# Kernel tuning notes

Measured on AMD Instinct MI355X. Metric: run time of the kernel, lower is better.

The kernel has to match this reference:

```python
import jax, jax.numpy as jnp
import numpy as np

EPS = 1e-5  # torch BatchNorm default eps


def _bn_relu(x, g, b, relu):
    # Training-mode BatchNorm1d over (N, C, L): stats over axes (0, 2).
    m = jnp.mean(x, axis=(0, 2), keepdims=True)
    v = jnp.var(x, axis=(0, 2), keepdims=True)
    y = (x - m) * jax.lax.rsqrt(v + EPS) * g[None, :, None] + b[None, :, None]
    return jax.nn.relu(y) if relu else y


def setup_inputs() -> dict:
    key = jax.random.key(0)
    k0, k1, k2 = jax.random.split(key, 3)
    N, C, H = 256, 512, 64  # batch, channels (inplanes==planes), spatial positions (mask_channel)
    x = jax.random.normal(k0, (N, C, H), dtype=jnp.float32)
    # LocallyConnected2d weights: torch shape (1, out, in, H, 1, k^2=1) -> (out, in, H)
    w1 = jax.random.normal(k1, (C, C, H), dtype=jnp.float32) * 0.02
    w2 = jax.random.normal(k2, (C, C, H), dtype=jnp.float32) * 0.02
    g1 = jnp.ones((C,), jnp.float32)
    b1 = jnp.zeros((C,), jnp.float32)
    g2 = jnp.ones((C,), jnp.float32)
    b2 = jnp.zeros((C,), jnp.float32)
    return {"x": x, "w1": w1, "g1": g1, "b1": b1, "w2": w2, "g2": g2, "b2": b2}


def reference(x, w1, g1, b1, w2, g2, b2):
    # conv1: locally-connected 1x1 -> per-position matmul over channels
    out = jnp.einsum('nch,och->noh', x, w1)          # (N, C, H)
    out = _bn_relu(out, g1, b1, relu=True)
    # conv2
    out = jnp.einsum('nch,och->noh', out, w2)
    out = _bn_relu(out, g2, b2, relu=False)
    # residual add (downsample is None) + final relu
    return jax.nn.relu(out + x)
```

## Files before the change

### kernel.cpp

```cpp
#include <hip/hip_runtime.h>
#include <stdint.h>

typedef float  f32x4  __attribute__((ext_vector_type(4)));
typedef __bf16 bf16x8 __attribute__((ext_vector_type(8)));
typedef __bf16 bf16x4 __attribute__((ext_vector_type(4)));

#define N_ 256
#define C_ 512
#define H_ 64
#define RS_ 32768

__device__ __forceinline__ uint32_t pack_bf16x2(float a, float b) {
  const uint16_t ua = __builtin_bit_cast(uint16_t, (__bf16)a);
  const uint16_t ub = __builtin_bit_cast(uint16_t, (__bf16)b);
  return (uint32_t)ua | ((uint32_t)ub << 16);
}

__global__ __launch_bounds__(256) void k_prep(const float* __restrict__ x,
                                              const float* __restrict__ w1,
                                              const float* __restrict__ w2,
                                              __bf16* __restrict__ xT,
                                              __bf16* __restrict__ w1T,
                                              __bf16* __restrict__ w2T,
                                              float* __restrict__ stats) {
  __shared__ uint32_t tile[256][33];
  const int t  = threadIdx.x;
  const int by = blockIdx.y;
  if (by == 0 && blockIdx.x == 0) {
#pragma unroll
    for (int i = 0; i < 8; ++i) stats[i * 256 + t] = 0.f;
  }
  const float* src;
  __bf16* dst;
  int p;
  if (by < 256)      { src = x;  dst = xT;  p = by; }
  else if (by < 768) { src = w1; dst = w1T; p = by - 256; }
  else               { src = w2; dst = w2T; p = by - 768; }
  const int ch0 = blockIdx.x * 256;
  const float* sbase = src + ((size_t)p * 512 + ch0) * 64;

#pragma unroll
  for (int j = 0; j < 16; ++j) {
    const int fidx = j * 256 + t;
    const int c = fidx >> 4, hq = fidx & 15;
    const float4 v = *reinterpret_cast<const float4*>(sbase + c * 64 + hq * 4);
    tile[c][hq * 2]     = pack_bf16x2(v.x, v.y);
    tile[c][hq * 2 + 1] = pack_bf16x2(v.z, v.w);
  }
  __syncthreads();

  __bf16* dbase = dst + (size_t)p * RS_ + ch0;
#pragma unroll
  for (int j = 0; j < 8; ++j) {
    const int ci = j * 256 + t;
    const int cb = ci & 31, h = ci >> 5;
    const int hm = h >> 1;
    const bool odd = (h & 1) != 0;
    uint32_t W[8];
#pragma unroll
    for (int i = 0; i < 8; ++i) W[i] = tile[cb * 8 + i][hm];
    uint4 o;
    uint32_t* op = reinterpret_cast<uint32_t*>(&o);
#pragma unroll
    for (int k = 0; k < 4; ++k) {
      const uint32_t wa = W[2 * k], wb = W[2 * k + 1];
      op[k] = odd ? ((wa >> 16) | (wb & 0xFFFF0000u))
                  : ((wa & 0xFFFFu) | (wb << 16));
    }
    *reinterpret_cast<uint4*>(dbase + (size_t)h * 512 + cb * 8) = o;
  }
}

template <bool BN_A>
__global__ __launch_bounds__(256, 2) void k_gemm(
    const __bf16* __restrict__ A,
    const __bf16* __restrict__ B,
    __bf16* __restrict__ Co,
    const float* __restrict__ sum_in, const float* __restrict__ sq_in,
    const float* __restrict__ g, const float* __restrict__ bb,
    float* __restrict__ sum_out, float* __restrict__ sq_out) {
  const int wkid = (blockIdx.x & 7) * 64 + (blockIdx.x >> 3);
  const int h  = wkid >> 3;
  const int tm = (wkid >> 2) & 1, tn = wkid & 3;
  const int m0 = tm * 128, n0 = tn * 128;
  const __bf16* Ah = A + (size_t)m0 * RS_ + (size_t)h * C_;
  const __bf16* Bh = B + (size_t)n0 * RS_ + (size_t)h * C_;
  __shared__ __bf16 As[2][128 * 64];
  __shared__ __bf16 Bs[2][128 * 64];
  __shared__ float a_lds[512], c_lds[512];
  const int tid  = threadIdx.x;
  const int lane = tid & 63, wid = tid >> 6;
  const int wr = wid >> 1, wc = wid & 1;
  const int lrow8 = lane >> 3;
  const int swz   = (lane & 7) ^ lrow8;

  if (BN_A) {
#pragma unroll
    for (int ch = tid; ch < 512; ch += 256) {
      const float m    = sum_in[ch] * (1.f / 16384.f);
      const float var  = fmaxf(0.f, sq_in[ch] * (1.f / 16384.f) - m * m);
      const float aa   = g[ch] * rsqrtf(var + 1e-5f);
      a_lds[ch] = aa;
      c_lds[ch] = bb[ch] - m * aa;
    }
    __syncthreads();
  }

  auto stage_b = [&](int buf, int kt) {
#pragma unroll
    for (int i = 0; i < 4; ++i) {
      const int rbase = wid * 32 + i * 8;
      const __bf16* gb = Bh + (size_t)(rbase + lrow8) * RS_ + kt * 64 + swz * 8;
      __builtin_amdgcn_global_load_lds(
          (const __attribute__((address_space(1))) void*)gb,
          (__attribute__((address_space(3))) void*)(&Bs[buf][rbase * 64]), 16, 0, 0);
    }
  };
  auto stage_a = [&](int buf, int kt) {
#pragma unroll
    for (int i = 0; i < 4; ++i) {
      const int rbase = wid * 32 + i * 8;
      const __bf16* ga = Ah + (size_t)(rbase + lrow8) * RS_ + kt * 64 + swz * 8;
      __builtin_amdgcn_global_load_lds(
          (const __attribute__((address_space(1))) void*)ga,
          (__attribute__((address_space(3))) void*)(&As[buf][rbase * 64]), 16, 0, 0);
    }
  };
  const int lr32 = tid >> 3, cch = tid & 7;
  auto load_a = [&](bf16x8* v, int kt) {
#pragma unroll
    for (int i = 0; i < 4; ++i)
      v[i] = *reinterpret_cast<const bf16x8*>(
          Ah + (size_t)(i * 32 + lr32) * RS_ + kt * 64 + cch * 8);
  };
  auto bn_write = [&](const bf16x8* v, int buf, int kt) {
    const int cg = kt * 64 + cch * 8;
    const f32x4 s0 = *reinterpret_cast<const f32x4*>(&a_lds[cg]);
    const f32x4 s1 = *reinterpret_cast<const f32x4*>(&a_lds[cg + 4]);
    const f32x4 h0 = *reinterpret_cast<const f32x4*>(&c_lds[cg]);
    const f32x4 h1 = *reinterpret_cast<const f32x4*>(&c_lds[cg + 4]);
#pragma unroll
    for (int i = 0; i < 4; ++i) {
      const int row = i * 32 + lr32;
      bf16x8 y;
#pragma unroll
      for (int e = 0; e < 4; ++e) {
        y[e]     = (__bf16)fmaxf(0.f, fmaf((float)v[i][e],     s0[e], h0[e]));
        y[e + 4] = (__bf16)fmaxf(0.f, fmaf((float)v[i][e + 4], s1[e], h1[e]));
      }
      const int boff = row * 128 + ((cch * 16) ^ ((row & 7) << 4));
      *reinterpret_cast<bf16x8*>(reinterpret_cast<char*>(&As[buf][0]) + boff) = y;
    }
  };

  f32x4 acc[4][4] = {};
  const int fr = lane & 15, kc = lane >> 4;
  auto compute = [&](int buf) {
#pragma unroll
    for (int kk = 0; kk < 2; ++kk) {
      bf16x8 af[4], bfq[4];
#pragma unroll
      for (int mf = 0; mf < 4; ++mf) {
        const int row  = wr * 64 + mf * 16 + fr;
        const int boff = row * 128 + ((kk * 64 + kc * 16) ^ ((row & 7) << 4));
        af[mf] = *reinterpret_cast<const bf16x8*>(
            reinterpret_cast<const char*>(&As[buf][0]) + boff);
      }
#pragma unroll
      for (int nf = 0; nf < 4; ++nf) {
        const int row  = wc * 64 + nf * 16 + fr;
        const int boff = row * 128 + ((kk * 64 + kc * 16) ^ ((row & 7) << 4));
        bfq[nf] = *reinterpret_cast<const bf16x8*>(
            reinterpret_cast<const char*>(&Bs[buf][0]) + boff);
      }
#pragma unroll
      for (int mf = 0; mf < 4; ++mf)
#pragma unroll
        for (int nf = 0; nf < 4; ++nf)
          acc[mf][nf] = __builtin_amdgcn_mfma_f32_16x16x32_bf16(af[mf], bfq[nf], acc[mf][nf], 0, 0, 0);
    }
  };

  if (BN_A) {
    bf16x8 v0[4];
    load_a(v0, 0);
    bn_write(v0, 0, 0);
  } else {
    stage_a(0, 0);
  }
  stage_b(0, 0);
  __syncthreads();

  int buf = 0;
  for (int kt = 0; kt < 8; ++kt) {
    bf16x8 vn[4];
    if (kt < 7) {
      stage_b(buf ^ 1, kt + 1);
      if (!BN_A) stage_a(buf ^ 1, kt + 1);
      else       load_a(vn, kt + 1);
    }
    compute(buf);
    if (BN_A && kt < 7) bn_write(vn, buf ^ 1, kt + 1);
    __syncthreads();
    buf ^= 1;
  }

  const int rq = (lane >> 4) * 4;
#pragma unroll
  for (int nf = 0; nf < 4; ++nf) {
    const int oc = n0 + wc * 64 + nf * 16 + fr;
    float s = 0.f, s2 = 0.f;
#pragma unroll
    for (int mf = 0; mf < 4; ++mf) {
      const int rb = m0 + wr * 64 + mf * 16 + rq;
      f32x4 v = acc[mf][nf];
#pragma unroll
      for (int j = 0; j < 4; ++j) {
        const float f = v[j];
        Co[(size_t)(rb + j) * RS_ + (size_t)h * C_ + oc] = (__bf16)f;
        s += f;
        s2 += f * f;
      }
    }
    s  += __shfl_xor(s, 16);  s  += __shfl_xor(s, 32);
    s2 += __shfl_xor(s2, 16); s2 += __shfl_xor(s2, 32);
    if (lane < 16) {
      atomicAdd(&sum_out[oc], s);
      atomicAdd(&sq_out[oc], s2);
    }
  }
}

__global__ __launch_bounds__(256) void k_finalize(const __bf16* __restrict__ t2,
                                                  const float* __restrict__ x,
                                                  const float* __restrict__ sum2,
                                                  const float* __restrict__ sq2,
                                                  const float* __restrict__ g2,
                                                  const float* __restrict__ b2,
                                                  float* __restrict__ out) {
  __shared__ float tile[64][65];
  __shared__ float a2s[64], c2s[64];
  const int n  = blockIdx.y;
  const int o0 = blockIdx.x * 64;
  const int t  = threadIdx.x;
  if (t < 64) {
    const int o = o0 + t;
    const float m    = sum2[o] * (1.f / 16384.f);
    const float var  = fmaxf(0.f, sq2[o] * (1.f / 16384.f) - m * m);
    const float a    = g2[o] * rsqrtf(var + 1e-5f);
    a2s[t] = a;
    c2s[t] = b2[o] - m * a;
  }
  const __bf16* tb = t2 + (size_t)n * RS_ + o0;
#pragma unroll
  for (int j = 0; j < 4; ++j) {
    const int hh = j * 16 + (t >> 4);
    const int ol = (t & 15) * 4;
    const bf16x4 v = *reinterpret_cast<const bf16x4*>(tb + (size_t)hh * 512 + ol);
#pragma unroll
    for (int e = 0; e < 4; ++e) tile[hh][ol + e] = (float)v[e];
  }
  __syncthreads();
  const int ol = t >> 2;
  const int hb = (t & 3) * 16;
  const int o  = o0 + ol;
  const float a = a2s[ol], c = c2s[ol];
  const float4* xp = reinterpret_cast<const float4*>(x + ((size_t)n * C_ + o) * H_ + hb);
  float4* op = reinterpret_cast<float4*>(out + ((size_t)n * C_ + o) * H_ + hb);
#pragma unroll
  for (int i4 = 0; i4 < 4; ++i4) {
    const float4 xv = xp[i4];
    float4 r;
    r.x = fmaxf(0.f, fmaf(a, tile[hb + i4 * 4 + 0][ol], c) + xv.x);
    r.y = fmaxf(0.f, fmaf(a, tile[hb + i4 * 4 + 1][ol], c) + xv.y);
    r.z = fmaxf(0.f, fmaf(a, tile[hb + i4 * 4 + 2][ol], c) + xv.z);
    r.w = fmaxf(0.f, fmaf(a, tile[hb + i4 * 4 + 3][ol], c) + xv.w);
    op[i4] = r;
  }
}

extern "C" void kernel_launch(void* const* d_in, const int* in_sizes, int n_in,
                              void* d_out, int out_size, void* d_ws, size_t ws_size,
                              hipStream_t stream) {
  const float* x  = (const float*)d_in[0];
  const float* w1 = (const float*)d_in[1];
  const float* g1 = (const float*)d_in[2];
  const float* b1 = (const float*)d_in[3];
  const float* w2 = (const float*)d_in[4];
  const float* g2 = (const float*)d_in[5];
  const float* b2 = (const float*)d_in[6];
  float* out = (float*)d_out;

  char* ws = (char*)d_ws;
  float* stats = (float*)ws;
  float* sum1 = stats,        *sq1 = stats + 512;
  float* sum2 = stats + 1024, *sq2 = stats + 1536;
  const size_t MB = (size_t)1 << 20;
  __bf16* xT  = (__bf16*)(ws + 64 * 1024);
  __bf16* w1T = (__bf16*)(ws + 64 * 1024 + 16 * MB);
  __bf16* w2T = (__bf16*)(ws + 64 * 1024 + 48 * MB);
  __bf16* t1T = (__bf16*)(ws + 64 * 1024 + 80 * MB);
  __bf16* t2T = (__bf16*)(ws + 64 * 1024 + 96 * MB);

  k_prep<<<dim3(2, 1280), 256, 0, stream>>>(x, w1, w2, xT, w1T, w2T, stats);

  k_gemm<false><<<512, 256, 0, stream>>>(xT, w1T, t1T, nullptr, nullptr,
                                         nullptr, nullptr, sum1, sq1);
  k_gemm<true><<<512, 256, 0, stream>>>(t1T, w2T, t2T, sum1, sq1, g1, b1,
                                        sum2, sq2);

  k_finalize<<<dim3(8, 256), 256, 0, stream>>>(t2T, x, sum2, sq2, g2, b2, out);
}
```

Measured before the change: 107.7 us.

## Restructure prep transpose as persistent per-wave tasks and split GEMM kernels

The prep kernel becomes a grid of 640 blocks whose waves each loop over small 64-channel tasks, staging into a private LDS slice with no block-level barriers. The old version used 2560 blocks with 256-channel tiles and a __syncthreads. The GEMM is moved into a device-function body with two separate wrapper kernels, so the kernel without BN no longer allocates the BN scale LDS arrays. The aim is to cut launch and barrier overhead in the transpose and reduce LDS footprint. The risk is less memory-level parallelism per wave in the prep stage.

```diff
diff --git a/kernel.cpp b/kernel.cpp
--- a/kernel.cpp
+++ b/kernel.cpp
@@ -16,79 +16,79 @@
   return (uint32_t)ua | ((uint32_t)ub << 16);
 }
 
-__global__ __launch_bounds__(256) void k_prep(const float* __restrict__ x,
-                                              const float* __restrict__ w1,
-                                              const float* __restrict__ w2,
-                                              __bf16* __restrict__ xT,
-                                              __bf16* __restrict__ w1T,
-                                              __bf16* __restrict__ w2T,
-                                              float* __restrict__ stats) {
-  __shared__ uint32_t tile[256][33];
-  const int t  = threadIdx.x;
-  const int by = blockIdx.y;
-  if (by == 0 && blockIdx.x == 0) {
+__global__ __launch_bounds__(256) void k_prep_all(const float* __restrict__ x,
+                                                  const float* __restrict__ w1,
+                                                  const float* __restrict__ w2,
+                                                  __bf16* __restrict__ xT,
+                                                  __bf16* __restrict__ w1T,
+                                                  __bf16* __restrict__ w2T,
+                                                  float* __restrict__ stats) {
+  __shared__ uint32_t lds[4][64 * 33];
+  const int t = threadIdx.x, wid = t >> 6, l = t & 63;
+  if (blockIdx.x == 0) {
 #pragma unroll
     for (int i = 0; i < 8; ++i) stats[i * 256 + t] = 0.f;
   }
-  const float* src;
-  __bf16* dst;
-  int p;
-  if (by < 256)      { src = x;  dst = xT;  p = by; }
-  else if (by < 768) { src = w1; dst = w1T; p = by - 256; }
-  else               { src = w2; dst = w2T; p = by - 768; }
-  const int ch0 = blockIdx.x * 256;
-  const float* sbase = src + ((size_t)p * 512 + ch0) * 64;
-
-#pragma unroll
-  for (int j = 0; j < 16; ++j) {
-    const int fidx = j * 256 + t;
-    const int c = fidx >> 4, hq = fidx & 15;
-    const float4 v = *reinterpret_cast<const float4*>(sbase + c * 64 + hq * 4);
-    tile[c][hq * 2]     = pack_bf16x2(v.x, v.y);
-    tile[c][hq * 2 + 1] = pack_bf16x2(v.z, v.w);
-  }
-  __syncthreads();
-
-  __bf16* dbase = dst + (size_t)p * RS_ + ch0;
-#pragma unroll
-  for (int j = 0; j < 8; ++j) {
-    const int ci = j * 256 + t;
-    const int cb = ci & 31, h = ci >> 5;
-    const int hm = h >> 1;
-    const bool odd = (h & 1) != 0;
-    uint32_t W[8];
-#pragma unroll
-    for (int i = 0; i < 8; ++i) W[i] = tile[cb * 8 + i][hm];
-    uint4 o;
-    uint32_t* op = reinterpret_cast<uint32_t*>(&o);
-#pragma unroll
-    for (int k = 0; k < 4; ++k) {
-      const uint32_t wa = W[2 * k], wb = W[2 * k + 1];
-      op[k] = odd ? ((wa >> 16) | (wb & 0xFFFF0000u))
-                  : ((wa & 0xFFFFu) | (wb << 16));
-    }
-    *reinterpret_cast<uint4*>(dbase + (size_t)h * 512 + cb * 8) = o;
+  uint32_t* my = lds[wid];
+  const int gw = blockIdx.x * 4 + wid;
+
+  for (int task = gw; task < 10240; task += 2560) {
+    const float* src;
+    __bf16* dst;
+    int u;
+    if (task < 2048)      { src = x;  dst = xT;  u = task; }
+    else if (task < 6144) { src = w1; dst = w1T; u = task - 2048; }
+    else                  { src = w2; dst = w2T; u = task - 6144; }
+    const int p = u >> 3, cb = u & 7;
+    const float* sb = src + ((size_t)p * 512 + cb * 64) * 64;
+
+#pragma unroll
+    for (int i = 0; i < 16; ++i) {
+      const int c  = i * 4 + (l >> 4);
+      const int hq = l & 15;
+      const float4 v = *reinterpret_cast<const float4*>(sb + c * 64 + hq * 4);
+      my[c * 33 + 2 * hq]     = pack_bf16x2(v.x, v.y);
+      my[c * 33 + 2 * hq + 1] = pack_bf16x2(v.z, v.w);
+    }
+
+    __bf16* db = dst + (size_t)p * RS_ + cb * 64;
+#pragma unroll
+    for (int s = 0; s < 8; ++s) {
+      const int h  = s * 8 + (l >> 3);
+      const int a  = l & 7;
+      const int hm = h >> 1;
+      const bool odd = (h & 1) != 0;
+      uint32_t W[8];
+#pragma unroll
+      for (int i = 0; i < 8; ++i) W[i] = my[(a * 8 + i) * 33 + hm];
+      uint4 o;
+      uint32_t* op = reinterpret_cast<uint32_t*>(&o);
+#pragma unroll
+      for (int k = 0; k < 4; ++k) {
+        const uint32_t wa = W[2 * k], wb = W[2 * k + 1];
+        op[k] = odd ? ((wa >> 16) | (wb & 0xFFFF0000u))
+                    : ((wa & 0xFFFFu) | (wb << 16));
+      }
+      *reinterpret_cast<uint4*>(db + (size_t)h * 512 + a * 8) = o;
+    }
   }
 }
 
 template <bool BN_A>
-__global__ __launch_bounds__(256, 2) void k_gemm(
-    const __bf16* __restrict__ A,
-    const __bf16* __restrict__ B,
+__device__ __forceinline__ void gemm_body(
+    const __bf16* __restrict__ A, const __bf16* __restrict__ B,
     __bf16* __restrict__ Co,
     const float* __restrict__ sum_in, const float* __restrict__ sq_in,
     const float* __restrict__ g, const float* __restrict__ bb,
-    float* __restrict__ sum_out, float* __restrict__ sq_out) {
-  const int wkid = (blockIdx.x & 7) * 64 + (blockIdx.x >> 3);
+    float* __restrict__ sum_out, float* __restrict__ sq_out,
+    int gblk, int tid, __bf16* AsB, __bf16* BsB,
+    float* a_lds, float* c_lds) {
+  const int wkid = (gblk & 7) * 64 + (gblk >> 3);
   const int h  = wkid >> 3;
   const int tm = (wkid >> 2) & 1, tn = wkid & 3;
   const int m0 = tm * 128, n0 = tn * 128;
   const __bf16* Ah = A + (size_t)m0 * RS_ + (size_t)h * C_;
   const __bf16* Bh = B + (size_t)n0 * RS_ + (size_t)h * C_;
-  __shared__ __bf16 As[2][128 * 64];
-  __shared__ __bf16 Bs[2][128 * 64];
-  __shared__ float a_lds[512], c_lds[512];
-  const int tid  = threadIdx.x;
   const int lane = tid & 63, wid = tid >> 6;
   const int wr = wid >> 1, wc = wid & 1;
   const int lrow8 = lane >> 3;
@@ -113,7 +113,8 @@
       const __bf16* gb = Bh + (size_t)(rbase + lrow8) * RS_ + kt * 64 + swz * 8;
       __builtin_amdgcn_global_load_lds(
           (const __attribute__((address_space(1))) void*)gb,
-          (__attribute__((address_space(3))) void*)(&Bs[buf][rbase * 64]), 16, 0, 0);
+          (__attribute__((address_space(3))) void*)(BsB + buf * 8192 + rbase * 64),
+          16, 0, 0);
     }
   };
   auto stage_a = [&](int buf, int kt) {
@@ -123,7 +124,8 @@
       const __bf16* ga = Ah + (size_t)(rbase + lrow8) * RS_ + kt * 64 + swz * 8;
       __builtin_amdgcn_global_load_lds(
           (const __attribute__((address_space(1))) void*)ga,
-          (__attribute__((address_space(3))) void*)(&As[buf][rbase * 64]), 16, 0, 0);
+          (__attribute__((address_space(3))) void*)(AsB + buf * 8192 + rbase * 64),
+          16, 0, 0);
     }
   };
   const int lr32 = tid >> 3, cch = tid & 7;
@@ -149,7 +151,7 @@
         y[e + 4] = (__bf16)fmaxf(0.f, fmaf((float)v[i][e + 4], s1[e], h1[e]));
       }
       const int boff = row * 128 + ((cch * 16) ^ ((row & 7) << 4));
-      *reinterpret_cast<bf16x8*>(reinterpret_cast<char*>(&As[buf][0]) + boff) = y;
+      *reinterpret_cast<bf16x8*>(reinterpret_cast<char*>(AsB + buf * 8192) + boff) = y;
     }
   };
 
@@ -164,14 +166,14 @@
         const int row  = wr * 64 + mf * 16 + fr;
         const int boff = row * 128 + ((kk * 64 + kc * 16) ^ ((row & 7) << 4));
         af[mf] = *reinterpret_cast<const bf16x8*>(
-            reinterpret_cast<const char*>(&As[buf][0]) + boff);
+            reinterpret_cast<const char*>(AsB + buf * 8192) + boff);
       }
 #pragma unroll
       for (int nf = 0; nf < 4; ++nf) {
         const int row  = wc * 64 + nf * 16 + fr;
         const int boff = row * 128 + ((kk * 64 + kc * 16) ^ ((row & 7) << 4));
         bfq[nf] = *reinterpret_cast<const bf16x8*>(
-            reinterpret_cast<const char*>(&Bs[buf][0]) + boff);
+            reinterpret_cast<const char*>(BsB + buf * 8192) + boff);
       }
 #pragma unroll
       for (int mf = 0; mf < 4; ++mf)
@@ -229,6 +231,31 @@
       atomicAdd(&sq_out[oc], s2);
     }
   }
+}
+
+__global__ __launch_bounds__(256, 2) void k_gemm1(
+    const __bf16* __restrict__ xT, const __bf16* __restrict__ w1T,
+    __bf16* __restrict__ t1T,
+    float* __restrict__ sum1, float* __restrict__ sq1) {
+  __shared__ __bf16 As[2][8192];
+  __shared__ __bf16 Bs[2][8192];
+  gemm_body<false>(xT, w1T, t1T, nullptr, nullptr, nullptr, nullptr,
+                   sum1, sq1, (int)blockIdx.x, (int)threadIdx.x,
+                   &As[0][0], &Bs[0][0], nullptr, nullptr);
+}
+
+__global__ __launch_bounds__(256, 2) void k_gemm2(
+    const __bf16* __restrict__ t1T, const __bf16* __restrict__ w2T,
+    __bf16* __restrict__ t2T,
+    const float* __restrict__ sum1, const float* __restrict__ sq1,
+    const float* __restrict__ g1, const float* __restrict__ b1,
+    float* __restrict__ sum2, float* __restrict__ sq2) {
+  __shared__ __bf16 As[2][8192];
+  __shared__ __bf16 Bs[2][8192];
+  __shared__ float a_lds[512], c_lds[512];
+  gemm_body<true>(t1T, w2T, t2T, sum1, sq1, g1, b1, sum2, sq2,
+                  (int)blockIdx.x, (int)threadIdx.x,
+                  &As[0][0], &Bs[0][0], a_lds, c_lds);
 }
 
 __global__ __launch_bounds__(256) void k_finalize(const __bf16* __restrict__ t2,
@@ -302,12 +329,8 @@
   __bf16* t1T = (__bf16*)(ws + 64 * 1024 + 80 * MB);
   __bf16* t2T = (__bf16*)(ws + 64 * 1024 + 96 * MB);
 
-  k_prep<<<dim3(2, 1280), 256, 0, stream>>>(x, w1, w2, xT, w1T, w2T, stats);
-
-  k_gemm<false><<<512, 256, 0, stream>>>(xT, w1T, t1T, nullptr, nullptr,
-                                         nullptr, nullptr, sum1, sq1);
-  k_gemm<true><<<512, 256, 0, stream>>>(t1T, w2T, t2T, sum1, sq1, g1, b1,
-                                        sum2, sq2);
-
+  k_prep_all<<<640, 256, 0, stream>>>(x, w1, w2, xT, w1T, w2T, stats);
+  k_gemm1<<<512, 256, 0, stream>>>(xT, w1T, t1T, sum1, sq1);
+  k_gemm2<<<512, 256, 0, stream>>>(t1T, w2T, t2T, sum1, sq1, g1, b1, sum2, sq2);
   k_finalize<<<dim3(8, 256), 256, 0, stream>>>(t2T, x, sum2, sq2, g2, b2, out);
 }
```

New measurement: 120.0 us. 1.11x slower.
